# Kernel tuning notes

Hardware: AMD Instinct MI355X
Metric: run time of the kernel (lower is better)

The kernel has to match this reference:

```python
import jax, jax.numpy as jnp
from jax import lax
import numpy as np

B, P, S, K = 16, 4096, 1024, 16   # clouds, points/cloud, fps samples/cloud (ratio 0.25), knn k
IN_F, OUT_F = 256, 512
EPS = 1e-5


def setup_inputs() -> dict:
    key = jax.random.key(0)
    k1, k2, k3 = jax.random.split(key, 3)
    features = jax.random.normal(k1, (B * P, IN_F), jnp.float32)
    positions = jax.random.normal(k2, (B * P, 3), jnp.float32)
    batch = jnp.repeat(jnp.arange(B, dtype=jnp.int32), P)
    W = jax.random.normal(k3, (IN_F, OUT_F), jnp.float32) / np.sqrt(IN_F)
    b = jnp.zeros((OUT_F,), jnp.float32)
    gamma = jnp.ones((OUT_F,), jnp.float32)
    beta = jnp.zeros((OUT_F,), jnp.float32)
    return {"features": features, "positions": positions, "batch": batch,
            "W": W, "b": b, "gamma": gamma, "beta": beta}


def _fps_local(pos):
    """Farthest point sampling on one cloud. pos: [P,3] -> [S] int32 local indices.
    Deterministic start at index 0 (torch_cluster fps with random_start disabled)."""
    def step(carry, _):
        min_d, last = carry
        d = jnp.sum((pos - pos[last]) ** 2, axis=-1)
        min_d = jnp.minimum(min_d, d)
        nxt = jnp.argmax(min_d).astype(jnp.int32)
        return (min_d, nxt), last
    init = (jnp.full((pos.shape[0],), jnp.inf, pos.dtype), jnp.int32(0))
    _, idx = lax.scan(step, init, None, length=S)
    return idx


def _knn_local(q, x):
    """K nearest neighbors of queries q [S,F] among x [P,F] (squared L2). -> [S,K] int32."""
    d = jnp.sum(q * q, -1, keepdims=True) - 2.0 * (q @ x.T) + jnp.sum(x * x, -1)
    _, idx = lax.top_k(-d, K)
    return idx


def reference(features, positions, batch, W, b, gamma, beta):
    pos_b = positions.reshape(B, P, 3)
    feat_b = features.reshape(B, P, IN_F)

    # --- FPS on positions, per cloud ---
    fps_loc = jax.vmap(_fps_local)(pos_b)                      # [B,S]
    offsets = (jnp.arange(B, dtype=jnp.int32) * P)[:, None]    # [B,1]
    fps_glob = (fps_loc + offsets).reshape(-1)                 # [B*S]

    # --- MLP: Linear -> BatchNorm1d (training batch stats, biased var) -> ReLU ---
    h = features @ W + b                                       # [N,OUT_F]
    mu = jnp.mean(h, axis=0)
    var = jnp.var(h, axis=0)
    h = jax.nn.relu(gamma * (h - mu) * lax.rsqrt(var + EPS) + beta)

    # --- brute-force KNN in feature space: queries = features[fps_indices] ---
    q = jnp.take_along_axis(feat_b, fps_loc[..., None], axis=1)   # [B,S,IN_F]
    nn_loc = jax.vmap(_knn_local)(q, feat_b)                      # [B,S,K]
    nn_glob = nn_loc + offsets[..., None]                         # [B,S,K]

    # --- scatter max-pool: each query has exactly K neighbors -> max over K ---
    nb = h[nn_glob.reshape(-1)].reshape(B, S, K, OUT_F)
    new_features = jnp.max(nb, axis=2).reshape(B * S, OUT_F)

    return new_features, positions[fps_glob], batch[fps_glob]
```

## Files before the change

kernel.cpp:

```cpp
#include <hip/hip_runtime.h>
#include <cstddef>


#define TD_B   16
#define TD_P   4096
#define TD_S   1024
#define TD_K   16
#define TD_INF 256
#define TD_OUTF 512

typedef __attribute__((ext_vector_type(8))) _Float16 half8;
typedef __attribute__((ext_vector_type(4))) float    f32x4;
typedef __attribute__((ext_vector_type(2))) float    v2f;

__device__ __forceinline__ unsigned short f2bf(float x) {
    unsigned u = __float_as_uint(x);
    unsigned r = (u + 0x7fffu + ((u >> 16) & 1u)) >> 16;
    return (unsigned short)r;
}

struct FpsSm {
    float4 p4[TD_P];
    int    sel[TD_S];
    unsigned long long kw[2][8];
};
struct GemmSm {
    float As[16 * 260];
    float Bs[16 * 128];
};
union SmU {
    FpsSm f; GemmSm g;
    char pad_[84000];
};

#define TD_DPPSTEP(k, ctl, bc)                                                          \
    {                                                                                   \
        unsigned yh_ = (unsigned)__builtin_amdgcn_update_dpp(                           \
            0, (int)(unsigned)((k) >> 32), (ctl), 0xf, 0xf, (bc));                      \
        unsigned yl_ = (unsigned)__builtin_amdgcn_update_dpp(                           \
            0, (int)(unsigned)(k), (ctl), 0xf, 0xf, (bc));                              \
        unsigned long long y_ = ((unsigned long long)yh_ << 32) | yl_;                  \
        if (y_ > (k)) (k) = y_;                                                         \
    }

__global__ __launch_bounds__(512)
void td_fused(const float* __restrict__ feat, const float* __restrict__ pos,
              const float* __restrict__ W, const float* __restrict__ bias,
              unsigned short* __restrict__ H, int* __restrict__ FPSI,
              float* __restrict__ outP, float* __restrict__ outB,
              float* __restrict__ P1p, float* __restrict__ P2p) {
    __shared__ SmU sm;
    const int bx = blockIdx.x;
    const int t  = threadIdx.x;

    if (bx < 16) {
        __builtin_amdgcn_s_setprio(2);
        const int b = bx;
        const int w = t >> 6;
        v2f px[8], py[8], pz[8], md[8];
        int ni0[8], ni1[8];
        float lx = 0.0f, ly = 0.0f, lz = 0.0f;
        if (t < 256) {
#pragma unroll
            for (int j = 0; j < 8; ++j) {
                int p0 = j * 512 + t, p1 = p0 + 256;
                const float* q0 = pos + (size_t)(b * TD_P + p0) * 3;
                const float* q1 = pos + (size_t)(b * TD_P + p1) * 3;
                float x0 = q0[0], y0 = q0[1], z0 = q0[2];
                float x1 = q1[0], y1 = q1[1], z1 = q1[2];
                px[j] = (v2f){x0, x1}; py[j] = (v2f){y0, y1}; pz[j] = (v2f){z0, z1};
                sm.f.p4[p0] = make_float4(x0, y0, z0, 0.0f);
                sm.f.p4[p1] = make_float4(x1, y1, z1, 0.0f);
                md[j] = (v2f){__builtin_inff(), __builtin_inff()};
                ni0[j] = ~p0; ni1[j] = ~p1;
            }
            if (t == 0) sm.f.sel[0] = 0;
        }
        __syncthreads();
        if (t < 256) { float4 wp = sm.f.p4[0]; lx = wp.x; ly = wp.y; lz = wp.z; }
        for (int s = 0; s < TD_S - 1; ++s) {
            const int par = s & 1;
            if (t < 256) {
                double k[16];
                {
#pragma clang fp contract(off)
                    v2f l2x = (v2f){lx, lx}, l2y = (v2f){ly, ly}, l2z = (v2f){lz, lz};
#pragma unroll
                    for (int j = 0; j < 8; ++j) {
                        v2f dx = px[j] - l2x;
                        v2f dy = py[j] - l2y;
                        v2f dz = pz[j] - l2z;
                        v2f sx = dx * dx;
                        v2f sy = dy * dy;
                        v2f sz = dz * dz;
                        v2f dd = (sx + sy) + sz;
                        md[j] = __builtin_elementwise_min(md[j], dd);
                        k[2 * j]     = __hiloint2double(__float_as_int(md[j].x), ni0[j]);
                        k[2 * j + 1] = __hiloint2double(__float_as_int(md[j].y), ni1[j]);
                    }
                }
#pragma unroll
                for (int st = 8; st > 0; st >>= 1)
#pragma unroll
                    for (int i = 0; i < st; ++i) k[i] = fmax(k[i], k[i + st]);
                unsigned long long tk = (unsigned long long)__double_as_longlong(k[0]);
                TD_DPPSTEP(tk, 0x111, true)
                TD_DPPSTEP(tk, 0x112, true)
                TD_DPPSTEP(tk, 0x114, true)
                TD_DPPSTEP(tk, 0x118, true)
                TD_DPPSTEP(tk, 0x142, false)
                TD_DPPSTEP(tk, 0x143, false)
                if ((t & 63) == 63) sm.f.kw[par][w] = tk;
            }
            __syncthreads();
            if (t < 256) {
                const unsigned long long* kwp = sm.f.kw[par];
                double g01 = fmax(__longlong_as_double((long long)kwp[0]),
                                  __longlong_as_double((long long)kwp[1]));
                double g23 = fmax(__longlong_as_double((long long)kwp[2]),
                                  __longlong_as_double((long long)kwp[3]));
                double gk  = fmax(g01, g23);
                unsigned idx = ~(unsigned)__double2loint(gk);
                if (t == 0) sm.f.sel[s + 1] = (int)idx;
                float4 wp = sm.f.p4[idx];
                lx = wp.x; ly = wp.y; lz = wp.z;
            }
        }
        __syncthreads();
        for (int s = t; s < TD_S; s += 512) {
            int li = sm.f.sel[s];
            int og = b * TD_S + s;
            float4 wp = sm.f.p4[li];
            outP[og * 3 + 0] = wp.x;
            outP[og * 3 + 1] = wp.y;
            outP[og * 3 + 2] = wp.z;
            outB[og] = (float)b;
            FPSI[og] = b * TD_P + li;
        }
    } else {
        const int gb = bx - 16;
        const int mb = gb >> 2, nb = gb & 3;
        const int tm = t >> 4, tn = t & 15;
        float acc[8][8];
#pragma unroll
        for (int i = 0; i < 8; ++i)
#pragma unroll
            for (int j = 0; j < 8; ++j) acc[i][j] = 0.0f;
        float* As = sm.g.As;
        float* Bs = sm.g.Bs;
        for (int kc = 0; kc < 16; ++kc) {
#pragma unroll
            for (int p2 = 0; p2 < 2; ++p2) {
                int f4 = t + 512 * p2;
                int r = f4 >> 2, c4 = f4 & 3;
                float4 v = *(const float4*)&feat[(size_t)(mb * 256 + r) * 256 + kc * 16 + c4 * 4];
                As[(c4 * 4 + 0) * 260 + r] = v.x;
                As[(c4 * 4 + 1) * 260 + r] = v.y;
                As[(c4 * 4 + 2) * 260 + r] = v.z;
                As[(c4 * 4 + 3) * 260 + r] = v.w;
            }
            {
                int kk = t >> 5, n4 = t & 31;
                float4 v = *(const float4*)&W[(size_t)(kc * 16 + kk) * 512 + nb * 128 + n4 * 4];
                *(float4*)&Bs[kk * 128 + n4 * 4] = v;
            }
            __syncthreads();
#pragma unroll
            for (int kk = 0; kk < 16; ++kk) {
                float4 a0 = *(float4*)&As[kk * 260 + tm * 8];
                float4 a1 = *(float4*)&As[kk * 260 + tm * 8 + 4];
                float4 b0 = *(float4*)&Bs[kk * 128 + tn * 8];
                float4 b1 = *(float4*)&Bs[kk * 128 + tn * 8 + 4];
                float av[8] = {a0.x, a0.y, a0.z, a0.w, a1.x, a1.y, a1.z, a1.w};
                float bv2[8] = {b0.x, b0.y, b0.z, b0.w, b1.x, b1.y, b1.z, b1.w};
#pragma unroll
                for (int i = 0; i < 8; ++i)
#pragma unroll
                    for (int j = 0; j < 8; ++j)
                        acc[i][j] = fmaf(av[i], bv2[j], acc[i][j]);
            }
            __syncthreads();
        }
        float4 bb0 = *(const float4*)&bias[nb * 128 + tn * 8];
        float4 bb1 = *(const float4*)&bias[nb * 128 + tn * 8 + 4];
        float bsv[8] = {bb0.x, bb0.y, bb0.z, bb0.w, bb1.x, bb1.y, bb1.z, bb1.w};
        float s1v[8], s2v[8];
#pragma unroll
        for (int j = 0; j < 8; ++j) { s1v[j] = 0.0f; s2v[j] = 0.0f; }
#pragma unroll
        for (int i = 0; i < 8; ++i) {
            int row = mb * 256 + tm * 8 + i;
            float hh[8];
#pragma unroll
            for (int j = 0; j < 8; ++j) {
                hh[j] = acc[i][j] + bsv[j];
                s1v[j] += hh[j];
                s2v[j] = fmaf(hh[j], hh[j], s2v[j]);
            }
            uint4 pk;
            pk.x = (unsigned)f2bf(hh[0]) | ((unsigned)f2bf(hh[1]) << 16);
            pk.y = (unsigned)f2bf(hh[2]) | ((unsigned)f2bf(hh[3]) << 16);
            pk.z = (unsigned)f2bf(hh[4]) | ((unsigned)f2bf(hh[5]) << 16);
            pk.w = (unsigned)f2bf(hh[6]) | ((unsigned)f2bf(hh[7]) << 16);
            *(uint4*)&H[(size_t)row * 512 + nb * 128 + tn * 8] = pk;
        }
        float* red = As;
#pragma unroll
        for (int j = 0; j < 8; ++j) red[tm * 128 + tn * 8 + j] = s1v[j];
        __syncthreads();
        float r1 = 0.0f;
        if (t < 128) {
            for (int r = 0; r < 32; ++r) r1 += red[r * 128 + t];
        }
        __syncthreads();
#pragma unroll
        for (int j = 0; j < 8; ++j) red[tm * 128 + tn * 8 + j] = s2v[j];
        __syncthreads();
        if (t < 128) {
            float r2 = 0.0f;
            for (int r = 0; r < 32; ++r) r2 += red[r * 128 + t];
            P1p[mb * 512 + nb * 128 + t] = r1;
            P2p[mb * 512 + nb * 128 + t] = r2;
        }
    }
}

__global__ __launch_bounds__(512)
void td_bnfin(const float* __restrict__ P1p, const float* __restrict__ P2p,
              const float* __restrict__ gamma, const float* __restrict__ beta,
              float* __restrict__ SS) {
    const int ch = threadIdx.x;
    float s1 = 0, s2 = 0;
    for (int mb = 0; mb < 256; ++mb) {
        s1 += P1p[mb * 512 + ch];
        s2 += P2p[mb * 512 + ch];
    }
    const float invN = 1.0f / 65536.0f;
    float mu  = s1 * invN;
    float var = s2 * invN - mu * mu;
    float sc  = gamma[ch] * (1.0f / sqrtf(var + 1e-5f));
    float sh  = beta[ch] - mu * sc;
    SS[ch] = sc; SS[512 + ch] = sh;
}

__global__ __launch_bounds__(256, 2)
void td_knn2(const float* __restrict__ feat, const int* __restrict__ FPSI,
             float* __restrict__ PD, int* __restrict__ PI) {
    __shared__ union {
        _Float16 x[2][32][264];
        float    dt[128][33];
    } sm;
    __shared__ float QQs[128];
    __shared__ int   QR[128];
    __shared__ float xxs[32];

    const int bx = blockIdx.x, t = threadIdx.x;
    const int b = bx & 15, r2 = bx >> 4;
    const int qq8 = r2 >> 2, seg = r2 & 3;
    const int segbase = b * TD_P + seg * 1024;

    if (t < 128) QR[t] = FPSI[b * TD_S + qq8 * 128 + t];
    __syncthreads();

    const int w = t >> 6, lane = t & 63;
    const int m = lane & 15, quad = lane >> 4;

    half8 qh[2][8], ql[2][8];
#pragma unroll
    for (int qs = 0; qs < 2; ++qs) {
        const float* qp = feat + (size_t)QR[w * 32 + qs * 16 + m] * 256;
        float qq2 = 0.0f;
#pragma unroll
        for (int ks = 0; ks < 8; ++ks) {
            float4 f0 = *(const float4*)(qp + ks * 32 + quad * 8);
            float4 f1 = *(const float4*)(qp + ks * 32 + quad * 8 + 4);
            float fv[8] = {f0.x, f0.y, f0.z, f0.w, f1.x, f1.y, f1.z, f1.w};
            half8 h, l;
#pragma unroll
            for (int j = 0; j < 8; ++j) {
                _Float16 hv = (_Float16)fv[j];
                h[j] = hv;
                l[j] = (_Float16)(fv[j] - (float)hv);
                qq2 = fmaf(fv[j], fv[j], qq2);
            }
            qh[qs][ks] = h; ql[qs][ks] = l;
        }
        qq2 += __shfl_xor(qq2, 16, 64);
        qq2 += __shfl_xor(qq2, 32, 64);
        if (quad == 0) QQs[w * 32 + qs * 16 + m] = qq2;
    }

    float sd[16]; int si[16];
#pragma unroll
    for (int r = 0; r < 16; ++r) { sd[r] = __builtin_inff(); si[r] = 0x7fffffff; }

    const int xrow = t >> 3, part = t & 7;

    for (int ct = 0; ct < 32; ++ct) {
        __syncthreads();
        {
            const float* xp = feat + (size_t)(segbase + ct * 32 + xrow) * 256 + part * 32;
            float cn = 0.0f;
#pragma unroll
            for (int s2 = 0; s2 < 4; ++s2) {
                float4 f0 = *(const float4*)(xp + s2 * 8);
                float4 f1 = *(const float4*)(xp + s2 * 8 + 4);
                float fv[8] = {f0.x, f0.y, f0.z, f0.w, f1.x, f1.y, f1.z, f1.w};
                half8 h, l;
#pragma unroll
                for (int j = 0; j < 8; ++j) {
                    _Float16 hv = (_Float16)fv[j];
                    h[j] = hv;
                    l[j] = (_Float16)(fv[j] - (float)hv);
                    cn = fmaf(fv[j], fv[j], cn);
                }
                *(half8*)&sm.x[0][xrow][part * 32 + s2 * 8] = h;
                *(half8*)&sm.x[1][xrow][part * 32 + s2 * 8] = l;
            }
            cn += __shfl_xor(cn, 1, 64);
            cn += __shfl_xor(cn, 2, 64);
            cn += __shfl_xor(cn, 4, 64);
            if (part == 0) xxs[xrow] = cn;
        }
        __syncthreads();
        f32x4 acc[2][2];
        acc[0][0] = (f32x4)0.0f; acc[0][1] = (f32x4)0.0f;
        acc[1][0] = (f32x4)0.0f; acc[1][1] = (f32x4)0.0f;
#pragma unroll
        for (int ks = 0; ks < 8; ++ks) {
            half8 xh0 = *(half8*)&sm.x[0][m][ks * 32 + quad * 8];
            half8 xl0 = *(half8*)&sm.x[1][m][ks * 32 + quad * 8];
            half8 xh1 = *(half8*)&sm.x[0][16 + m][ks * 32 + quad * 8];
            half8 xl1 = *(half8*)&sm.x[1][16 + m][ks * 32 + quad * 8];
            acc[0][0] = __builtin_amdgcn_mfma_f32_16x16x32_f16(ql[0][ks], xh0, acc[0][0], 0, 0, 0);
            acc[0][1] = __builtin_amdgcn_mfma_f32_16x16x32_f16(ql[0][ks], xh1, acc[0][1], 0, 0, 0);
            acc[1][0] = __builtin_amdgcn_mfma_f32_16x16x32_f16(ql[1][ks], xh0, acc[1][0], 0, 0, 0);
            acc[1][1] = __builtin_amdgcn_mfma_f32_16x16x32_f16(ql[1][ks], xh1, acc[1][1], 0, 0, 0);
            acc[0][0] = __builtin_amdgcn_mfma_f32_16x16x32_f16(qh[0][ks], xl0, acc[0][0], 0, 0, 0);
            acc[0][1] = __builtin_amdgcn_mfma_f32_16x16x32_f16(qh[0][ks], xl1, acc[0][1], 0, 0, 0);
            acc[1][0] = __builtin_amdgcn_mfma_f32_16x16x32_f16(qh[1][ks], xl0, acc[1][0], 0, 0, 0);
            acc[1][1] = __builtin_amdgcn_mfma_f32_16x16x32_f16(qh[1][ks], xl1, acc[1][1], 0, 0, 0);
            acc[0][0] = __builtin_amdgcn_mfma_f32_16x16x32_f16(qh[0][ks], xh0, acc[0][0], 0, 0, 0);
            acc[0][1] = __builtin_amdgcn_mfma_f32_16x16x32_f16(qh[0][ks], xh1, acc[0][1], 0, 0, 0);
            acc[1][0] = __builtin_amdgcn_mfma_f32_16x16x32_f16(qh[1][ks], xh0, acc[1][0], 0, 0, 0);
            acc[1][1] = __builtin_amdgcn_mfma_f32_16x16x32_f16(qh[1][ks], xh1, acc[1][1], 0, 0, 0);
        }
        __syncthreads();
        {
            float xx0 = xxs[m];
            float xx1 = xxs[16 + m];
#pragma unroll
            for (int qs = 0; qs < 2; ++qs) {
                int qb = w * 32 + qs * 16 + quad * 4;
#pragma unroll
                for (int reg = 0; reg < 4; ++reg) {
                    float qq = QQs[qb + reg];
                    sm.dt[qb + reg][m]      = (qq - 2.0f * acc[qs][0][reg]) + xx0;
                    sm.dt[qb + reg][16 + m] = (qq - 2.0f * acc[qs][1][reg]) + xx1;
                }
            }
        }
        __syncthreads();
        if (t < 128) {
            const int ibase = segbase + ct * 32;
            for (int j = 0; j < 32; ++j) {
                float d = sm.dt[t][j];
                if (d < sd[15]) {
                    sd[15] = d; si[15] = ibase + j;
#pragma unroll
                    for (int r = 15; r > 0; --r) {
                        if (sd[r] < sd[r - 1]) {
                            float td2 = sd[r]; sd[r] = sd[r - 1]; sd[r - 1] = td2;
                            int ti = si[r]; si[r] = si[r - 1]; si[r - 1] = ti;
                        }
                    }
                }
            }
        }
    }
    if (t < 128) {
        size_t o = ((size_t)(b * TD_S + qq8 * 128 + t)) * 64 + seg * 16;
#pragma unroll
        for (int r = 0; r < 16; ++r) { PD[o + r] = sd[r]; PI[o + r] = si[r]; }
    }
}

__global__ __launch_bounds__(64)
void td_merge(const float* __restrict__ PD, const int* __restrict__ PI,
              int* __restrict__ NN) {
    __shared__ float ld_[64][65];
    __shared__ int   li_[64][65];
    const int bx = blockIdx.x, t = threadIdx.x;
    for (int j = 0; j < 64; ++j) {
        ld_[j][t] = PD[(size_t)bx * 4096 + j * 64 + t];
        li_[j][t] = PI[(size_t)bx * 4096 + j * 64 + t];
    }
    __syncthreads();
    int p[4] = {0, 0, 0, 0};
    int og = (bx * 64 + t) * TD_K;
    for (int r = 0; r < 16; ++r) {
        float bd = __builtin_inff(); int bi = 0x7fffffff; int bs = 0;
#pragma unroll
        for (int s = 0; s < 4; ++s) {
            if (p[s] < 16) {
                float d = ld_[t][s * 16 + p[s]];
                int   i = li_[t][s * 16 + p[s]];
                if (d < bd || (d == bd && i < bi)) { bd = d; bi = i; bs = s; }
            }
        }
        p[bs]++;
        NN[og + r] = bi;
    }
}

__global__ __launch_bounds__(256)
void td_maxpool(const unsigned short* __restrict__ H, const int* __restrict__ NN,
                const float* __restrict__ SS, float* __restrict__ outF) {
    __shared__ int nbr[64];
    const int bx = blockIdx.x, t = threadIdx.x;
    const int cloud = bx & 15, blk = bx >> 4;
    const int qbase = cloud * 1024 + blk * 4;
    if (t < 64) nbr[t] = NN[(size_t)qbase * 16 + t];
    __syncthreads();
    float sc0 = SS[2 * t], sc1 = SS[2 * t + 1];
    float sh0 = SS[512 + 2 * t], sh1 = SS[512 + 2 * t + 1];
#pragma unroll
    for (int qi = 0; qi < 4; ++qi) {
        float m0 = 0.0f, m1 = 0.0f;
#pragma unroll
        for (int k = 0; k < 16; ++k) {
            int row = nbr[qi * 16 + k];
            unsigned u = ((const unsigned*)(H + (size_t)row * 512))[t];
            float lo = __uint_as_float(u << 16);
            float hi = __uint_as_float(u & 0xffff0000u);
            m0 = fmaxf(m0, fmaf(sc0, lo, sh0));
            m1 = fmaxf(m1, fmaf(sc1, hi, sh1));
        }
        float2 o; o.x = m0; o.y = m1;
        *(float2*)&outF[(size_t)(qbase + qi) * 512 + 2 * t] = o;
    }
}

extern "C" void kernel_launch(void* const* d_in, const int* in_sizes, int n_in,
                              void* d_out, int out_size, void* d_ws, size_t ws_size,
                              hipStream_t stream) {
    const float* feat  = (const float*)d_in[0];
    const float* pos   = (const float*)d_in[1];
    const float* W     = (const float*)d_in[3];
    const float* bias  = (const float*)d_in[4];
    const float* gamma = (const float*)d_in[5];
    const float* beta  = (const float*)d_in[6];

    char* ws = (char*)d_ws;
    unsigned short* H = (unsigned short*)ws;
    int*   FPSI= (int*)  (ws + 67108864);
    int*   NN  = (int*)  (ws + 67174400);
    float* P1p = (float*)(ws + 68222976);
    float* P2p = (float*)(ws + 68747264);
    float* SS  = (float*)(ws + 69271552);
    float* PD  = (float*)(ws + 69275648);
    int*   PI  = (int*)  (ws + 73469952);

    float* outF = (float*)d_out;
    float* outP = outF + (size_t)TD_B * TD_S * TD_OUTF;
    float* outB = outP + (size_t)TD_B * TD_S * 3;

    td_fused  <<<1040, 512, 0, stream>>>(feat, pos, W, bias, H, FPSI, outP, outB, P1p, P2p);
    td_bnfin  <<<1, 512, 0, stream>>>(P1p, P2p, gamma, beta, SS);
    td_knn2   <<<512, 256, 0, stream>>>(feat, FPSI, PD, PI);
    td_merge  <<<256, 64, 0, stream>>>(PD, PI, NN);
    td_maxpool<<<TD_B * 256, 256, 0, stream>>>(H, NN, SS, outF);
}
```

Measured before the change: 1.081 ms.

## Fold BN finalize into knn kernel and merge step into maxpool, use double DPP max

Removes two kernel launches. The BatchNorm statistics finalization now runs as an extra block of the knn kernel, and the 4-way partial top-k merge now runs inside the maxpool kernel. The FPS wave reduction also uses a double fmax on DPP-shuffled halves in place of a 64-bit integer compare. This trades launch overhead and the NN round trip for redundant per-block merge work done by only 4 threads, and the BN block adds a serial tail to the knn grid.

```diff
diff --git a/kernel.cpp b/kernel.cpp
--- a/kernel.cpp
+++ b/kernel.cpp
@@ -33,14 +33,14 @@
     char pad_[84000];
 };
 
-#define TD_DPPSTEP(k, ctl, bc)                                                          \
+#define TD_DPPSTEPD(kd_, ctl, bc)                                                       \
     {                                                                                   \
+        long long ki_ = __double_as_longlong(kd_);                                      \
         unsigned yh_ = (unsigned)__builtin_amdgcn_update_dpp(                           \
-            0, (int)(unsigned)((k) >> 32), (ctl), 0xf, 0xf, (bc));                      \
+            0, (int)((unsigned long long)ki_ >> 32), (ctl), 0xf, 0xf, (bc));            \
         unsigned yl_ = (unsigned)__builtin_amdgcn_update_dpp(                           \
-            0, (int)(unsigned)(k), (ctl), 0xf, 0xf, (bc));                              \
-        unsigned long long y_ = ((unsigned long long)yh_ << 32) | yl_;                  \
-        if (y_ > (k)) (k) = y_;                                                         \
+            0, (int)(unsigned)(unsigned long long)ki_, (ctl), 0xf, 0xf, (bc));          \
+        kd_ = fmax(kd_, __hiloint2double((int)yh_, (int)yl_));                          \
     }
 
 __global__ __launch_bounds__(512)
@@ -103,23 +103,21 @@
                 for (int st = 8; st > 0; st >>= 1)
 #pragma unroll
                     for (int i = 0; i < st; ++i) k[i] = fmax(k[i], k[i + st]);
-                unsigned long long tk = (unsigned long long)__double_as_longlong(k[0]);
-                TD_DPPSTEP(tk, 0x111, true)
-                TD_DPPSTEP(tk, 0x112, true)
-                TD_DPPSTEP(tk, 0x114, true)
-                TD_DPPSTEP(tk, 0x118, true)
-                TD_DPPSTEP(tk, 0x142, false)
-                TD_DPPSTEP(tk, 0x143, false)
-                if ((t & 63) == 63) sm.f.kw[par][w] = tk;
+                double tk = k[0];
+                TD_DPPSTEPD(tk, 0x111, true)
+                TD_DPPSTEPD(tk, 0x112, true)
+                TD_DPPSTEPD(tk, 0x114, true)
+                TD_DPPSTEPD(tk, 0x118, true)
+                TD_DPPSTEPD(tk, 0x142, false)
+                TD_DPPSTEPD(tk, 0x143, false)
+                if ((t & 63) == 63)
+                    sm.f.kw[par][w] = (unsigned long long)__double_as_longlong(tk);
             }
             __syncthreads();
             if (t < 256) {
-                const unsigned long long* kwp = sm.f.kw[par];
-                double g01 = fmax(__longlong_as_double((long long)kwp[0]),
-                                  __longlong_as_double((long long)kwp[1]));
-                double g23 = fmax(__longlong_as_double((long long)kwp[2]),
-                                  __longlong_as_double((long long)kwp[3]));
-                double gk  = fmax(g01, g23);
+                const double2* kd = (const double2*)sm.f.kw[par];
+                double2 va = kd[0], vb = kd[1];
+                double gk = fmax(fmax(va.x, va.y), fmax(vb.x, vb.y));
                 unsigned idx = ~(unsigned)__double2loint(gk);
                 if (t == 0) sm.f.sel[s + 1] = (int)idx;
                 float4 wp = sm.f.p4[idx];
@@ -225,27 +223,12 @@
     }
 }
 
-__global__ __launch_bounds__(512)
-void td_bnfin(const float* __restrict__ P1p, const float* __restrict__ P2p,
-              const float* __restrict__ gamma, const float* __restrict__ beta,
-              float* __restrict__ SS) {
-    const int ch = threadIdx.x;
-    float s1 = 0, s2 = 0;
-    for (int mb = 0; mb < 256; ++mb) {
-        s1 += P1p[mb * 512 + ch];
-        s2 += P2p[mb * 512 + ch];
-    }
-    const float invN = 1.0f / 65536.0f;
-    float mu  = s1 * invN;
-    float var = s2 * invN - mu * mu;
-    float sc  = gamma[ch] * (1.0f / sqrtf(var + 1e-5f));
-    float sh  = beta[ch] - mu * sc;
-    SS[ch] = sc; SS[512 + ch] = sh;
-}
-
 __global__ __launch_bounds__(256, 2)
 void td_knn2(const float* __restrict__ feat, const int* __restrict__ FPSI,
-             float* __restrict__ PD, int* __restrict__ PI) {
+             float* __restrict__ PD, int* __restrict__ PI,
+             const float* __restrict__ P1p, const float* __restrict__ P2p,
+             const float* __restrict__ gamma, const float* __restrict__ beta,
+             float* __restrict__ SS) {
     __shared__ union {
         _Float16 x[2][32][264];
         float    dt[128][33];
@@ -255,6 +238,22 @@
     __shared__ float xxs[32];
 
     const int bx = blockIdx.x, t = threadIdx.x;
+    if (bx == 512) {
+        for (int ch = t; ch < 512; ch += 256) {
+            float s1 = 0, s2 = 0;
+            for (int mb = 0; mb < 256; ++mb) {
+                s1 += P1p[mb * 512 + ch];
+                s2 += P2p[mb * 512 + ch];
+            }
+            const float invN = 1.0f / 65536.0f;
+            float mu  = s1 * invN;
+            float var = s2 * invN - mu * mu;
+            float sc  = gamma[ch] * (1.0f / sqrtf(var + 1e-5f));
+            float sh  = beta[ch] - mu * sc;
+            SS[ch] = sc; SS[512 + ch] = sh;
+        }
+        return;
+    }
     const int b = bx & 15, r2 = bx >> 4;
     const int qq8 = r2 >> 2, seg = r2 & 3;
     const int segbase = b * TD_P + seg * 1024;
@@ -385,42 +384,38 @@
     }
 }
 
-__global__ __launch_bounds__(64)
-void td_merge(const float* __restrict__ PD, const int* __restrict__ PI,
-              int* __restrict__ NN) {
-    __shared__ float ld_[64][65];
-    __shared__ int   li_[64][65];
-    const int bx = blockIdx.x, t = threadIdx.x;
-    for (int j = 0; j < 64; ++j) {
-        ld_[j][t] = PD[(size_t)bx * 4096 + j * 64 + t];
-        li_[j][t] = PI[(size_t)bx * 4096 + j * 64 + t];
-    }
-    __syncthreads();
-    int p[4] = {0, 0, 0, 0};
-    int og = (bx * 64 + t) * TD_K;
-    for (int r = 0; r < 16; ++r) {
-        float bd = __builtin_inff(); int bi = 0x7fffffff; int bs = 0;
-#pragma unroll
-        for (int s = 0; s < 4; ++s) {
-            if (p[s] < 16) {
-                float d = ld_[t][s * 16 + p[s]];
-                int   i = li_[t][s * 16 + p[s]];
-                if (d < bd || (d == bd && i < bi)) { bd = d; bi = i; bs = s; }
-            }
-        }
-        p[bs]++;
-        NN[og + r] = bi;
-    }
-}
-
 __global__ __launch_bounds__(256)
-void td_maxpool(const unsigned short* __restrict__ H, const int* __restrict__ NN,
-                const float* __restrict__ SS, float* __restrict__ outF) {
-    __shared__ int nbr[64];
+void td_maxpool(const unsigned short* __restrict__ H, const float* __restrict__ PD,
+                const int* __restrict__ PI, const float* __restrict__ SS,
+                float* __restrict__ outF) {
+    __shared__ float ld2[4][65];
+    __shared__ int   li2[4][65];
+    __shared__ int   nbr[64];
     const int bx = blockIdx.x, t = threadIdx.x;
     const int cloud = bx & 15, blk = bx >> 4;
     const int qbase = cloud * 1024 + blk * 4;
-    if (t < 64) nbr[t] = NN[(size_t)qbase * 16 + t];
+    {
+        int qi = t >> 6, j = t & 63;
+        ld2[qi][j] = PD[(size_t)(qbase + qi) * 64 + j];
+        li2[qi][j] = PI[(size_t)(qbase + qi) * 64 + j];
+    }
+    __syncthreads();
+    if (t < 4) {
+        int p[4] = {0, 0, 0, 0};
+        for (int r = 0; r < 16; ++r) {
+            float bd = __builtin_inff(); int bi = 0x7fffffff; int bs = 0;
+#pragma unroll
+            for (int s = 0; s < 4; ++s) {
+                if (p[s] < 16) {
+                    float d = ld2[t][s * 16 + p[s]];
+                    int   i = li2[t][s * 16 + p[s]];
+                    if (d < bd || (d == bd && i < bi)) { bd = d; bi = i; bs = s; }
+                }
+            }
+            p[bs]++;
+            nbr[t * 16 + r] = bi;
+        }
+    }
     __syncthreads();
     float sc0 = SS[2 * t], sc1 = SS[2 * t + 1];
     float sh0 = SS[512 + 2 * t], sh1 = SS[512 + 2 * t + 1];
@@ -454,20 +449,17 @@
     char* ws = (char*)d_ws;
     unsigned short* H = (unsigned short*)ws;
     int*   FPSI= (int*)  (ws + 67108864);
-    int*   NN  = (int*)  (ws + 67174400);
-    float* P1p = (float*)(ws + 68222976);
-    float* P2p = (float*)(ws + 68747264);
-    float* SS  = (float*)(ws + 69271552);
-    float* PD  = (float*)(ws + 69275648);
-    int*   PI  = (int*)  (ws + 73469952);
+    float* P1p = (float*)(ws + 67174400);
+    float* P2p = (float*)(ws + 67698688);
+    float* SS  = (float*)(ws + 68222976);
+    float* PD  = (float*)(ws + 68227072);
+    int*   PI  = (int*)  (ws + 72421376);
 
     float* outF = (float*)d_out;
     float* outP = outF + (size_t)TD_B * TD_S * TD_OUTF;
     float* outB = outP + (size_t)TD_B * TD_S * 3;
 
     td_fused  <<<1040, 512, 0, stream>>>(feat, pos, W, bias, H, FPSI, outP, outB, P1p, P2p);
-    td_bnfin  <<<1, 512, 0, stream>>>(P1p, P2p, gamma, beta, SS);
-    td_knn2   <<<512, 256, 0, stream>>>(feat, FPSI, PD, PI);
-    td_merge  <<<256, 64, 0, stream>>>(PD, PI, NN);
-    td_maxpool<<<TD_B * 256, 256, 0, stream>>>(H, NN, SS, outF);
+    td_knn2   <<<513, 256, 0, stream>>>(feat, FPSI, PD, PI, P1p, P2p, gamma, beta, SS);
+    td_maxpool<<<TD_B * 256, 256, 0, stream>>>(H, PD, PI, SS, outF);
 }
```

After: 1.043 ms. 3.5% less time.
